# Performance work log

Measured on AMD Instinct MI355X. Metric: run time of the kernel, lower is better.

Reference implementation:

```python
import jax, jax.numpy as jnp
import numpy as np

B, N, DIM = 4, 4096, 128
DEG, EXP = 2, 2
DE = DEG * EXP * DIM  # 512, expanded projection dim


def setup_inputs() -> dict:
    key = jax.random.key(0)
    ks = jax.random.split(key, 7)
    xq = jax.random.normal(ks[0], (B, N, DIM), dtype=jnp.float32)
    # causal 3D mask (batch, query_len, context_len)
    mask = jnp.broadcast_to(jnp.tril(jnp.ones((N, N), jnp.float32)), (B, N, N))
    sc_in = 1.0 / np.sqrt(DIM)
    sc_de = 1.0 / np.sqrt(DE)
    W_se = jax.random.normal(ks[1], (DE, DIM), jnp.float32) * sc_in
    b_se = jax.random.normal(ks[2], (DE,), jnp.float32) * 0.01
    W_po = jax.random.normal(ks[3], (DE, DIM), jnp.float32) * sc_in
    b_po = jax.random.normal(ks[4], (DE,), jnp.float32) * 0.01
    W_ag = jax.random.normal(ks[5], (DIM, DE), jnp.float32) * sc_de
    b_ag = jax.random.normal(ks[6], (DIM,), jnp.float32) * 0.01
    return {"xq": xq, "mask": mask, "W_se": W_se, "b_se": b_se,
            "W_po": W_po, "b_po": b_po, "W_ag": W_ag, "b_ag": b_ag}


def reference(xq, mask, W_se, b_se, W_po, b_po, W_ag, b_ag):
    # self-attention: xc = xq
    s = xq @ W_se.T + b_se                       # [B, N, DE]
    h = xq @ W_po.T + b_po                       # [B, N, DE]
    # po2: second-order polynomial expansion (exact-erf GELU, torch default)
    g = jax.nn.gelu(h, approximate=False)
    h1, h2 = jnp.split(g, 2, axis=-1)
    h = jnp.concatenate([h1, h2 * h1], axis=-1)  # [B, N, DE]
    # full_mask_mixer: masked aggregation + normalization
    agg = jnp.einsum('bnd,bmn->bmd', h, mask)    # [B, M, DE]
    agg = agg / (1e-7 + jnp.sum(mask, axis=2, keepdims=True))
    # polynomial selection: sigmoid gating
    o = jax.nn.sigmoid(s) * agg                  # [B, N, DE]
    return o @ W_ag.T + b_ag                     # [B, N, DIM]
```

## Files before the change

kernel.cpp:

```cpp
#include <hip/hip_runtime.h>
#include <math.h>

#define BB 4
#define NN 4096
#define DIM 128
#define DE 512
#define NTOK (BB * NN)
#define CH 32
#define NCHUNK (NN / CH)

typedef __attribute__((ext_vector_type(8))) short bf16x8;
typedef __attribute__((ext_vector_type(4))) float f32x4;

__device__ inline unsigned short f2bf(float f) {
    union { float f; unsigned int u; } v; v.f = f;
    unsigned int r = v.u + 0x7FFF + ((v.u >> 16) & 1);
    return (unsigned short)(r >> 16);
}
__device__ inline float bf2f(unsigned int h16) {
    union { unsigned int u; float f; } v; v.u = (h16 & 0xFFFFu) << 16;
    return v.f;
}
__device__ inline float gelu_erf(float x) {
    return 0.5f * x * (1.0f + erff(x * 0.70710678118654752f));
}
__device__ inline float sigmoidf(float x) {
    return 1.0f / (1.0f + expf(-x));
}

__global__ __launch_bounds__(256) void k0_convert(
    const float* __restrict__ A, const float* __restrict__ B,
    const float* __restrict__ C, unsigned short* __restrict__ w)
{
    int blk = blockIdx.x;
    const float* src = (blk < 64) ? A : ((blk < 128) ? B : C);
    unsigned short* dst = w + (size_t)(blk >> 6) * 65536;
    int base = (blk & 63) * 1024 + threadIdx.x * 4;
    float4 v = *(const float4*)&src[base];
    ushort4 o;
    o.x = f2bf(v.x); o.y = f2bf(v.y); o.z = f2bf(v.z); o.w = f2bf(v.w);
    *(ushort4*)&dst[base] = o;
}

#define XPAD 8
__global__ __launch_bounds__(256) void k1_proj(
    const float* __restrict__ xq,
    const unsigned short* __restrict__ wse, const unsigned short* __restrict__ wpo,
    const float* __restrict__ b_se, const float* __restrict__ b_po,
    unsigned short* __restrict__ hp, unsigned short* __restrict__ sg,
    float* __restrict__ S)
{
    __shared__ unsigned short xs[CH][DIM + XPAD];
    __shared__ float Ssum[DE];

    const int tid = threadIdx.x;
    const int blk = blockIdx.x;
    const int t0 = blk * CH;

    Ssum[tid] = 0.0f;
    Ssum[tid + 256] = 0.0f;

    for (int i = tid * 4; i < CH * DIM; i += 1024) {
        int tok = i >> 7, k = i & 127;
        float4 v = *(const float4*)&xq[(size_t)(t0 + tok) * DIM + k];
        ushort4 o;
        o.x = f2bf(v.x); o.y = f2bf(v.y); o.z = f2bf(v.z); o.w = f2bf(v.w);
        *(ushort4*)&xs[tok][k] = o;
    }
    __syncthreads();

    const int lane = tid & 63;
    const int w   = tid >> 6;
    const int tg  = w & 1;
    const int chf = w >> 1;
    const int l15 = lane & 15;
    const int q   = lane >> 4;

    bf16x8 af[4];
    #pragma unroll
    for (int ks = 0; ks < 4; ++ks)
        af[ks] = *(const bf16x8*)&xs[tg * 16 + l15][ks * 32 + q * 8];

    for (int m = 0; m < 2; ++m) {
        const unsigned short* W = m ? wpo : wse;
        const float* bias = m ? b_po : b_se;

        f32x4 accL[8], accH[8];
        #pragma unroll
        for (int i = 0; i < 8; ++i) {
            accL[i] = (f32x4){0.f, 0.f, 0.f, 0.f};
            accH[i] = (f32x4){0.f, 0.f, 0.f, 0.f};
        }

        #pragma unroll
        for (int ks = 0; ks < 4; ++ks) {
            #pragma unroll
            for (int i = 0; i < 8; ++i) {
                int colL = (chf * 8 + i) * 16 + l15;
                bf16x8 bL = *(const bf16x8*)&W[(size_t)colL * DIM + ks * 32 + q * 8];
                bf16x8 bH = *(const bf16x8*)&W[(size_t)(colL + 256) * DIM + ks * 32 + q * 8];
                accL[i] = __builtin_amdgcn_mfma_f32_16x16x32_bf16(af[ks], bL, accL[i], 0, 0, 0);
                accH[i] = __builtin_amdgcn_mfma_f32_16x16x32_bf16(af[ks], bH, accH[i], 0, 0, 0);
            }
        }

        #pragma unroll
        for (int i = 0; i < 8; ++i) {
            int colL = (chf * 8 + i) * 16 + l15;
            int colH = colL + 256;
            float bL = bias[colL], bH = bias[colH];
            if (m == 0) {
                #pragma unroll
                for (int r = 0; r < 4; ++r) {
                    size_t tok = (size_t)(t0 + tg * 16 + q * 4 + r);
                    sg[tok * DE + colL] = f2bf(sigmoidf(accL[i][r] + bL));
                    sg[tok * DE + colH] = f2bf(sigmoidf(accH[i][r] + bH));
                }
            } else {
                float sL = 0.f, sH = 0.f;
                #pragma unroll
                for (int r = 0; r < 4; ++r) {
                    size_t tok = (size_t)(t0 + tg * 16 + q * 4 + r);
                    float g1 = gelu_erf(accL[i][r] + bL);
                    float g2 = gelu_erf(accH[i][r] + bH);
                    float h2 = g2 * g1;
                    hp[tok * DE + colL] = f2bf(g1);
                    hp[tok * DE + colH] = f2bf(h2);
                    sL += g1; sH += h2;
                }
                sL += __shfl_xor(sL, 16); sL += __shfl_xor(sL, 32);
                sH += __shfl_xor(sH, 16); sH += __shfl_xor(sH, 32);
                if (q == 0) {
                    atomicAdd(&Ssum[colL], sL);
                    atomicAdd(&Ssum[colH], sH);
                }
            }
        }
    }
    __syncthreads();
    S[(size_t)blk * DE + tid]       = Ssum[tid];
    S[(size_t)blk * DE + tid + 256] = Ssum[tid + 256];
}

__global__ __launch_bounds__(256) void k2s_scan(float* __restrict__ S)
{
    const int b = blockIdx.x;
    const int d0 = threadIdx.x;
    float r0 = 0.f, r1 = 0.f;
    for (int c = 0; c < NCHUNK; ++c) {
        size_t idx = ((size_t)b * NCHUNK + c) * DE;
        float v0 = S[idx + d0];
        float v1 = S[idx + d0 + 256];
        S[idx + d0]       = r0;
        S[idx + d0 + 256] = r1;
        r0 += v0; r1 += v1;
    }
}

#define OPAD 8
__global__ __launch_bounds__(256) void k3_gate_out(
    const unsigned short* __restrict__ hp, const unsigned short* __restrict__ sg,
    const float* __restrict__ S, const unsigned short* __restrict__ wag,
    const float* __restrict__ b_ag, float* __restrict__ out)
{
    __shared__ unsigned short ot[CH][DE + OPAD];

    const int tid = threadIdx.x;
    const int blk = blockIdx.x;
    const int chunk = blk & (NCHUNK - 1);
    const int t0 = blk * CH;

    {
        const int d0 = tid * 2;
        float r0 = S[(size_t)blk * DE + d0];
        float r1 = S[(size_t)blk * DE + d0 + 1];
        const unsigned short* ph = hp + (size_t)t0 * DE + d0;
        const unsigned short* ps = sg + (size_t)t0 * DE + d0;
        for (int n = 0; n < CH; ++n) {
            unsigned int hv = *(const unsigned int*)ph;
            unsigned int sv = *(const unsigned int*)ps;
            r0 += bf2f(hv);
            r1 += bf2f(hv >> 16);
            float inv = 1.0f / ((float)(chunk * CH + n + 1) + 1e-7f);
            unsigned short o0 = f2bf(bf2f(sv) * (r0 * inv));
            unsigned short o1 = f2bf(bf2f(sv >> 16) * (r1 * inv));
            *(unsigned int*)&ot[n][d0] = (unsigned)o0 | ((unsigned)o1 << 16);
            ph += DE; ps += DE;
        }
    }
    __syncthreads();

    const int lane = tid & 63;
    const int w  = tid >> 6;
    const int tg = w & 1;
    const int cg = w >> 1;
    const int l15 = lane & 15;
    const int q   = lane >> 4;

    f32x4 acc[4];
    #pragma unroll
    for (int i = 0; i < 4; ++i) acc[i] = (f32x4){0.f, 0.f, 0.f, 0.f};

    for (int ks = 0; ks < 16; ++ks) {
        bf16x8 a = *(const bf16x8*)&ot[tg * 16 + l15][ks * 32 + q * 8];
        #pragma unroll
        for (int i = 0; i < 4; ++i) {
            int row = (cg * 4 + i) * 16 + l15;
            bf16x8 b = *(const bf16x8*)&wag[(size_t)row * DE + ks * 32 + q * 8];
            acc[i] = __builtin_amdgcn_mfma_f32_16x16x32_bf16(a, b, acc[i], 0, 0, 0);
        }
    }

    #pragma unroll
    for (int i = 0; i < 4; ++i) {
        int col = (cg * 4 + i) * 16 + l15;
        float bv = b_ag[col];
        #pragma unroll
        for (int r = 0; r < 4; ++r) {
            size_t tok = (size_t)(t0 + tg * 16 + q * 4 + r);
            out[tok * DIM + col] = acc[i][r] + bv;
        }
    }
}

extern "C" void kernel_launch(void* const* d_in, const int* in_sizes, int n_in,
                              void* d_out, int out_size, void* d_ws, size_t ws_size,
                              hipStream_t stream)
{
    const float* xq   = (const float*)d_in[0];
    const float* W_se = (const float*)d_in[2];
    const float* b_se = (const float*)d_in[3];
    const float* W_po = (const float*)d_in[4];
    const float* b_po = (const float*)d_in[5];
    const float* W_ag = (const float*)d_in[6];
    const float* b_ag = (const float*)d_in[7];
    float* out = (float*)d_out;

    unsigned short* wbf = (unsigned short*)d_ws;
    unsigned short* wse = wbf;
    unsigned short* wpo = wbf + 65536;
    unsigned short* wag = wbf + 131072;
    unsigned short* hp  = wbf + 196608;
    unsigned short* sg  = hp + (size_t)NTOK * DE;
    float* S            = (float*)(sg + (size_t)NTOK * DE);

    k0_convert<<<192, 256, 0, stream>>>(W_se, W_po, W_ag, wbf);
    k1_proj<<<NTOK / CH, 256, 0, stream>>>(xq, wse, wpo, b_se, b_po, hp, sg, S);
    k2s_scan<<<BB, 256, 0, stream>>>(S);
    k3_gate_out<<<NTOK / CH, 256, 0, stream>>>(hp, sg, S, wag, b_ag, out);
}
```

Measured before the change: 384.1 us.

## Recompute projections in fused output kernel instead of storing h and sigmoid intermediates

The first pass now computes only the GELU-expanded projection's per-chunk sums and no longer writes the full h and sigmoid tensors to global memory. The second kernel recomputes the po projection and computes the se projection and prefix sum in shared memory, then applies the gate and output GEMM. The separate scan kernel is removed: each block sums the earlier chunk sums itself. Weights are pre-packed into an MFMA-fragment-friendly layout so B-operand loads are contiguous. This trades roughly 32 MB of intermediate global traffic for a duplicated projection GEMM and a serial prefix loop of up to 127 chunks per block.

```diff
diff --git a/kernel.cpp b/kernel.cpp
--- a/kernel.cpp
+++ b/kernel.cpp
@@ -11,11 +11,12 @@
 
 typedef __attribute__((ext_vector_type(8))) short bf16x8;
 typedef __attribute__((ext_vector_type(4))) float f32x4;
-
-__device__ inline unsigned short f2bf(float f) {
+typedef unsigned short us;
+
+__device__ inline us f2bf(float f) {
     union { float f; unsigned int u; } v; v.f = f;
     unsigned int r = v.u + 0x7FFF + ((v.u >> 16) & 1);
-    return (unsigned short)(r >> 16);
+    return (us)(r >> 16);
 }
 __device__ inline float bf2f(unsigned int h16) {
     union { unsigned int u; float f; } v; v.u = (h16 & 0xFFFFu) << 16;
@@ -28,197 +29,262 @@
     return 1.0f / (1.0f + expf(-x));
 }
 
-__global__ __launch_bounds__(256) void k0_convert(
-    const float* __restrict__ A, const float* __restrict__ B,
-    const float* __restrict__ C, unsigned short* __restrict__ w)
+__global__ __launch_bounds__(256) void k0_pack(
+    const float* __restrict__ Wse, const float* __restrict__ Wpo,
+    const float* __restrict__ Wag, us* __restrict__ wp)
 {
-    int blk = blockIdx.x;
-    const float* src = (blk < 64) ? A : ((blk < 128) ? B : C);
-    unsigned short* dst = w + (size_t)(blk >> 6) * 65536;
-    int base = (blk & 63) * 1024 + threadIdx.x * 4;
-    float4 v = *(const float4*)&src[base];
-    ushort4 o;
-    o.x = f2bf(v.x); o.y = f2bf(v.y); o.z = f2bf(v.z); o.w = f2bf(v.w);
-    *(ushort4*)&dst[base] = o;
+    int gid = blockIdx.x * 256 + threadIdx.x;
+    int mat = gid >> 13;
+    int r   = gid & 8191;
+    int f   = r >> 6;
+    int lane = r & 63;
+    const float* src = (mat == 0) ? Wse : ((mat == 1) ? Wpo : Wag);
+    int K     = (mat == 2) ? DE : DIM;
+    int shift = (mat == 2) ? 4 : 2;
+    int ct = f >> shift;
+    int ks = f & ((1 << shift) - 1);
+    int col = ct * 16 + (lane & 15);
+    int k0  = ks * 32 + (lane >> 4) * 8;
+    const float* s = &src[(size_t)col * K + k0];
+    float4 a = *(const float4*)s;
+    float4 b = *(const float4*)(s + 4);
+    us o[8] = { f2bf(a.x), f2bf(a.y), f2bf(a.z), f2bf(a.w),
+                f2bf(b.x), f2bf(b.y), f2bf(b.z), f2bf(b.w) };
+    us* d = wp + (size_t)mat * 65536 + ((size_t)f * 64 + lane) * 8;
+    *(ushort4*)d       = *(ushort4*)&o[0];
+    *(ushort4*)(d + 4) = *(ushort4*)&o[4];
 }
 
 #define XPAD 8
-__global__ __launch_bounds__(256) void k1_proj(
-    const float* __restrict__ xq,
-    const unsigned short* __restrict__ wse, const unsigned short* __restrict__ wpo,
-    const float* __restrict__ b_se, const float* __restrict__ b_po,
-    unsigned short* __restrict__ hp, unsigned short* __restrict__ sg,
-    float* __restrict__ S)
+__global__ __launch_bounds__(256) void k1_chunksums(
+    const float* __restrict__ xq, const us* __restrict__ wpo,
+    const float* __restrict__ b_po, float* __restrict__ S)
 {
-    __shared__ unsigned short xs[CH][DIM + XPAD];
+    __shared__ us xs[CH][DIM + XPAD];
     __shared__ float Ssum[DE];
 
     const int tid = threadIdx.x;
     const int blk = blockIdx.x;
-    const int t0 = blk * CH;
-
-    Ssum[tid] = 0.0f;
-    Ssum[tid + 256] = 0.0f;
+    const size_t t0 = (size_t)blk * CH;
+
+    Ssum[tid] = 0.f;
+    Ssum[tid + 256] = 0.f;
 
     for (int i = tid * 4; i < CH * DIM; i += 1024) {
         int tok = i >> 7, k = i & 127;
-        float4 v = *(const float4*)&xq[(size_t)(t0 + tok) * DIM + k];
-        ushort4 o;
-        o.x = f2bf(v.x); o.y = f2bf(v.y); o.z = f2bf(v.z); o.w = f2bf(v.w);
+        float4 v = *(const float4*)&xq[(t0 + tok) * DIM + k];
+        ushort4 o = { f2bf(v.x), f2bf(v.y), f2bf(v.z), f2bf(v.w) };
         *(ushort4*)&xs[tok][k] = o;
     }
     __syncthreads();
 
-    const int lane = tid & 63;
-    const int w   = tid >> 6;
-    const int tg  = w & 1;
-    const int chf = w >> 1;
-    const int l15 = lane & 15;
-    const int q   = lane >> 4;
+    const int lane = tid & 63, w = tid >> 6;
+    const int tg = w & 1, chf = w >> 1;
+    const int l15 = lane & 15, q = lane >> 4;
 
     bf16x8 af[4];
     #pragma unroll
     for (int ks = 0; ks < 4; ++ks)
         af[ks] = *(const bf16x8*)&xs[tg * 16 + l15][ks * 32 + q * 8];
 
-    for (int m = 0; m < 2; ++m) {
-        const unsigned short* W = m ? wpo : wse;
-        const float* bias = m ? b_po : b_se;
-
+    f32x4 accL[8], accH[8];
+    #pragma unroll
+    for (int i = 0; i < 8; ++i) {
+        accL[i] = (f32x4){0.f, 0.f, 0.f, 0.f};
+        accH[i] = (f32x4){0.f, 0.f, 0.f, 0.f};
+    }
+
+    #pragma unroll
+    for (int ks = 0; ks < 4; ++ks) {
+        #pragma unroll
+        for (int i = 0; i < 8; ++i) {
+            int ctL = chf * 8 + i;
+            bf16x8 bL = *(const bf16x8*)&wpo[(size_t)((ctL * 4 + ks) * 64 + lane) * 8];
+            bf16x8 bH = *(const bf16x8*)&wpo[(size_t)(((ctL + 16) * 4 + ks) * 64 + lane) * 8];
+            accL[i] = __builtin_amdgcn_mfma_f32_16x16x32_bf16(af[ks], bL, accL[i], 0, 0, 0);
+            accH[i] = __builtin_amdgcn_mfma_f32_16x16x32_bf16(af[ks], bH, accH[i], 0, 0, 0);
+        }
+    }
+
+    #pragma unroll
+    for (int i = 0; i < 8; ++i) {
+        int colL = (chf * 8 + i) * 16 + l15;
+        int colH = colL + 256;
+        float bL = b_po[colL], bH = b_po[colH];
+        float sL = 0.f, sH = 0.f;
+        #pragma unroll
+        for (int r = 0; r < 4; ++r) {
+            float g1 = gelu_erf(accL[i][r] + bL);
+            float g2 = gelu_erf(accH[i][r] + bH);
+            sL += g1;
+            sH += g2 * g1;
+        }
+        sL += __shfl_xor(sL, 16); sL += __shfl_xor(sL, 32);
+        sH += __shfl_xor(sH, 16); sH += __shfl_xor(sH, 32);
+        if (q == 0) {
+            atomicAdd(&Ssum[colL], sL);
+            atomicAdd(&Ssum[colH], sH);
+        }
+    }
+    __syncthreads();
+    S[(size_t)blk * DE + tid]       = Ssum[tid];
+    S[(size_t)blk * DE + tid + 256] = Ssum[tid + 256];
+}
+
+#define OPAD 8
+__global__ __launch_bounds__(256) void k3_fused(
+    const float* __restrict__ xq, const us* __restrict__ wse,
+    const us* __restrict__ wpo, const us* __restrict__ wag,
+    const float* __restrict__ b_se, const float* __restrict__ b_po,
+    const float* __restrict__ S, const float* __restrict__ b_ag,
+    float* __restrict__ out)
+{
+    __shared__ us xs[CH][DIM + XPAD];
+    __shared__ us ht[CH][DE + OPAD];
+    __shared__ float pre[DE];
+
+    const int tid = threadIdx.x;
+    const int blk = blockIdx.x;
+    const int c = blk & (NCHUNK - 1);
+    const int b = blk >> 7;
+    const size_t t0 = (size_t)blk * CH;
+
+    for (int i = tid * 4; i < CH * DIM; i += 1024) {
+        int tok = i >> 7, k = i & 127;
+        float4 v = *(const float4*)&xq[(t0 + tok) * DIM + k];
+        ushort4 o = { f2bf(v.x), f2bf(v.y), f2bf(v.z), f2bf(v.w) };
+        *(ushort4*)&xs[tok][k] = o;
+    }
+    {
+        int d = tid * 2;
+        float r0 = 0.f, r1 = 0.f;
+        const float* p = &S[((size_t)b * NCHUNK) * DE + d];
+        for (int cc = 0; cc < c; ++cc) {
+            float2 v = *(const float2*)p;
+            r0 += v.x; r1 += v.y;
+            p += DE;
+        }
+        pre[d] = r0; pre[d + 1] = r1;
+    }
+    __syncthreads();
+
+    const int lane = tid & 63, w = tid >> 6;
+    const int tg = w & 1, chf = w >> 1;
+    const int l15 = lane & 15, q = lane >> 4;
+
+    bf16x8 af[4];
+    #pragma unroll
+    for (int ks = 0; ks < 4; ++ks)
+        af[ks] = *(const bf16x8*)&xs[tg * 16 + l15][ks * 32 + q * 8];
+
+    {
         f32x4 accL[8], accH[8];
         #pragma unroll
         for (int i = 0; i < 8; ++i) {
             accL[i] = (f32x4){0.f, 0.f, 0.f, 0.f};
             accH[i] = (f32x4){0.f, 0.f, 0.f, 0.f};
         }
-
         #pragma unroll
         for (int ks = 0; ks < 4; ++ks) {
             #pragma unroll
             for (int i = 0; i < 8; ++i) {
-                int colL = (chf * 8 + i) * 16 + l15;
-                bf16x8 bL = *(const bf16x8*)&W[(size_t)colL * DIM + ks * 32 + q * 8];
-                bf16x8 bH = *(const bf16x8*)&W[(size_t)(colL + 256) * DIM + ks * 32 + q * 8];
+                int ctL = chf * 8 + i;
+                bf16x8 bL = *(const bf16x8*)&wpo[(size_t)((ctL * 4 + ks) * 64 + lane) * 8];
+                bf16x8 bH = *(const bf16x8*)&wpo[(size_t)(((ctL + 16) * 4 + ks) * 64 + lane) * 8];
                 accL[i] = __builtin_amdgcn_mfma_f32_16x16x32_bf16(af[ks], bL, accL[i], 0, 0, 0);
                 accH[i] = __builtin_amdgcn_mfma_f32_16x16x32_bf16(af[ks], bH, accH[i], 0, 0, 0);
             }
         }
-
         #pragma unroll
         for (int i = 0; i < 8; ++i) {
             int colL = (chf * 8 + i) * 16 + l15;
             int colH = colL + 256;
-            float bL = bias[colL], bH = bias[colH];
-            if (m == 0) {
-                #pragma unroll
-                for (int r = 0; r < 4; ++r) {
-                    size_t tok = (size_t)(t0 + tg * 16 + q * 4 + r);
-                    sg[tok * DE + colL] = f2bf(sigmoidf(accL[i][r] + bL));
-                    sg[tok * DE + colH] = f2bf(sigmoidf(accH[i][r] + bH));
-                }
-            } else {
-                float sL = 0.f, sH = 0.f;
-                #pragma unroll
-                for (int r = 0; r < 4; ++r) {
-                    size_t tok = (size_t)(t0 + tg * 16 + q * 4 + r);
-                    float g1 = gelu_erf(accL[i][r] + bL);
-                    float g2 = gelu_erf(accH[i][r] + bH);
-                    float h2 = g2 * g1;
-                    hp[tok * DE + colL] = f2bf(g1);
-                    hp[tok * DE + colH] = f2bf(h2);
-                    sL += g1; sH += h2;
-                }
-                sL += __shfl_xor(sL, 16); sL += __shfl_xor(sL, 32);
-                sH += __shfl_xor(sH, 16); sH += __shfl_xor(sH, 32);
-                if (q == 0) {
-                    atomicAdd(&Ssum[colL], sL);
-                    atomicAdd(&Ssum[colH], sH);
-                }
-            }
-        }
-    }
-    __syncthreads();
-    S[(size_t)blk * DE + tid]       = Ssum[tid];
-    S[(size_t)blk * DE + tid + 256] = Ssum[tid + 256];
-}
-
-__global__ __launch_bounds__(256) void k2s_scan(float* __restrict__ S)
-{
-    const int b = blockIdx.x;
-    const int d0 = threadIdx.x;
-    float r0 = 0.f, r1 = 0.f;
-    for (int c = 0; c < NCHUNK; ++c) {
-        size_t idx = ((size_t)b * NCHUNK + c) * DE;
-        float v0 = S[idx + d0];
-        float v1 = S[idx + d0 + 256];
-        S[idx + d0]       = r0;
-        S[idx + d0 + 256] = r1;
-        r0 += v0; r1 += v1;
-    }
-}
-
-#define OPAD 8
-__global__ __launch_bounds__(256) void k3_gate_out(
-    const unsigned short* __restrict__ hp, const unsigned short* __restrict__ sg,
-    const float* __restrict__ S, const unsigned short* __restrict__ wag,
-    const float* __restrict__ b_ag, float* __restrict__ out)
-{
-    __shared__ unsigned short ot[CH][DE + OPAD];
-
-    const int tid = threadIdx.x;
-    const int blk = blockIdx.x;
-    const int chunk = blk & (NCHUNK - 1);
-    const int t0 = blk * CH;
-
-    {
-        const int d0 = tid * 2;
-        float r0 = S[(size_t)blk * DE + d0];
-        float r1 = S[(size_t)blk * DE + d0 + 1];
-        const unsigned short* ph = hp + (size_t)t0 * DE + d0;
-        const unsigned short* ps = sg + (size_t)t0 * DE + d0;
+            float bL = b_po[colL], bH = b_po[colH];
+            #pragma unroll
+            for (int r = 0; r < 4; ++r) {
+                int tok = tg * 16 + q * 4 + r;
+                float g1 = gelu_erf(accL[i][r] + bL);
+                float g2 = gelu_erf(accH[i][r] + bH);
+                ht[tok][colL] = f2bf(g1);
+                ht[tok][colH] = f2bf(g2 * g1);
+            }
+        }
+    }
+    __syncthreads();
+
+    {
+        int d = tid * 2;
+        float r0 = pre[d], r1 = pre[d + 1];
+        #pragma unroll 4
         for (int n = 0; n < CH; ++n) {
-            unsigned int hv = *(const unsigned int*)ph;
-            unsigned int sv = *(const unsigned int*)ps;
+            unsigned hv = *(unsigned*)&ht[n][d];
             r0 += bf2f(hv);
             r1 += bf2f(hv >> 16);
-            float inv = 1.0f / ((float)(chunk * CH + n + 1) + 1e-7f);
-            unsigned short o0 = f2bf(bf2f(sv) * (r0 * inv));
-            unsigned short o1 = f2bf(bf2f(sv >> 16) * (r1 * inv));
-            *(unsigned int*)&ot[n][d0] = (unsigned)o0 | ((unsigned)o1 << 16);
-            ph += DE; ps += DE;
-        }
-    }
-    __syncthreads();
-
-    const int lane = tid & 63;
-    const int w  = tid >> 6;
-    const int tg = w & 1;
-    const int cg = w >> 1;
-    const int l15 = lane & 15;
-    const int q   = lane >> 4;
-
-    f32x4 acc[4];
-    #pragma unroll
-    for (int i = 0; i < 4; ++i) acc[i] = (f32x4){0.f, 0.f, 0.f, 0.f};
-
-    for (int ks = 0; ks < 16; ++ks) {
-        bf16x8 a = *(const bf16x8*)&ot[tg * 16 + l15][ks * 32 + q * 8];
+            float inv = 1.0f / ((float)(c * CH + n + 1) + 1e-7f);
+            *(unsigned*)&ht[n][d] = (unsigned)f2bf(r0 * inv)
+                                  | ((unsigned)f2bf(r1 * inv) << 16);
+        }
+    }
+    __syncthreads();
+
+    {
+        f32x4 accL[8], accH[8];
+        #pragma unroll
+        for (int i = 0; i < 8; ++i) {
+            accL[i] = (f32x4){0.f, 0.f, 0.f, 0.f};
+            accH[i] = (f32x4){0.f, 0.f, 0.f, 0.f};
+        }
+        #pragma unroll
+        for (int ks = 0; ks < 4; ++ks) {
+            #pragma unroll
+            for (int i = 0; i < 8; ++i) {
+                int ctL = chf * 8 + i;
+                bf16x8 bL = *(const bf16x8*)&wse[(size_t)((ctL * 4 + ks) * 64 + lane) * 8];
+                bf16x8 bH = *(const bf16x8*)&wse[(size_t)(((ctL + 16) * 4 + ks) * 64 + lane) * 8];
+                accL[i] = __builtin_amdgcn_mfma_f32_16x16x32_bf16(af[ks], bL, accL[i], 0, 0, 0);
+                accH[i] = __builtin_amdgcn_mfma_f32_16x16x32_bf16(af[ks], bH, accH[i], 0, 0, 0);
+            }
+        }
+        #pragma unroll
+        for (int i = 0; i < 8; ++i) {
+            int colL = (chf * 8 + i) * 16 + l15;
+            int colH = colL + 256;
+            float bL = b_se[colL], bH = b_se[colH];
+            #pragma unroll
+            for (int r = 0; r < 4; ++r) {
+                int tok = tg * 16 + q * 4 + r;
+                float aggL = bf2f((unsigned)ht[tok][colL]);
+                float aggH = bf2f((unsigned)ht[tok][colH]);
+                ht[tok][colL] = f2bf(sigmoidf(accL[i][r] + bL) * aggL);
+                ht[tok][colH] = f2bf(sigmoidf(accH[i][r] + bH) * aggH);
+            }
+        }
+    }
+    __syncthreads();
+
+    {
+        f32x4 acc[4];
+        #pragma unroll
+        for (int i = 0; i < 4; ++i) acc[i] = (f32x4){0.f, 0.f, 0.f, 0.f};
+
+        for (int ks = 0; ks < 16; ++ks) {
+            bf16x8 a = *(const bf16x8*)&ht[tg * 16 + l15][ks * 32 + q * 8];
+            #pragma unroll
+            for (int i = 0; i < 4; ++i) {
+                int ct = chf * 4 + i;
+                bf16x8 bb = *(const bf16x8*)&wag[(size_t)((ct * 16 + ks) * 64 + lane) * 8];
+                acc[i] = __builtin_amdgcn_mfma_f32_16x16x32_bf16(a, bb, acc[i], 0, 0, 0);
+            }
+        }
         #pragma unroll
         for (int i = 0; i < 4; ++i) {
-            int row = (cg * 4 + i) * 16 + l15;
-            bf16x8 b = *(const bf16x8*)&wag[(size_t)row * DE + ks * 32 + q * 8];
-            acc[i] = __builtin_amdgcn_mfma_f32_16x16x32_bf16(a, b, acc[i], 0, 0, 0);
-        }
-    }
-
-    #pragma unroll
-    for (int i = 0; i < 4; ++i) {
-        int col = (cg * 4 + i) * 16 + l15;
-        float bv = b_ag[col];
-        #pragma unroll
-        for (int r = 0; r < 4; ++r) {
-            size_t tok = (size_t)(t0 + tg * 16 + q * 4 + r);
-            out[tok * DIM + col] = acc[i][r] + bv;
+            int col = (chf * 4 + i) * 16 + l15;
+            float bv = b_ag[col];
+            #pragma unroll
+            for (int r = 0; r < 4; ++r) {
+                size_t tok = t0 + tg * 16 + q * 4 + r;
+                out[tok * DIM + col] = acc[i][r] + bv;
+            }
         }
     }
 }
@@ -236,16 +302,14 @@
     const float* b_ag = (const float*)d_in[7];
     float* out = (float*)d_out;
 
-    unsigned short* wbf = (unsigned short*)d_ws;
-    unsigned short* wse = wbf;
-    unsigned short* wpo = wbf + 65536;
-    unsigned short* wag = wbf + 131072;
-    unsigned short* hp  = wbf + 196608;
-    unsigned short* sg  = hp + (size_t)NTOK * DE;
-    float* S            = (float*)(sg + (size_t)NTOK * DE);
-
-    k0_convert<<<192, 256, 0, stream>>>(W_se, W_po, W_ag, wbf);
-    k1_proj<<<NTOK / CH, 256, 0, stream>>>(xq, wse, wpo, b_se, b_po, hp, sg, S);
-    k2s_scan<<<BB, 256, 0, stream>>>(S);
-    k3_gate_out<<<NTOK / CH, 256, 0, stream>>>(hp, sg, S, wag, b_ag, out);
-}
+    us* wp  = (us*)d_ws;
+    us* wse = wp;
+    us* wpo = wp + 65536;
+    us* wag = wp + 131072;
+    float* S = (float*)(wp + 196608);
+
+    k0_pack<<<96, 256, 0, stream>>>(W_se, W_po, W_ag, wp);
+    k1_chunksums<<<NTOK / CH, 256, 0, stream>>>(xq, wpo, b_po, S);
+    k3_fused<<<NTOK / CH, 256, 0, stream>>>(xq, wse, wpo, wag,
+                                            b_se, b_po, S, b_ag, out);
+}
```

Result: slower. 426.6 us (+11.1%).
